# Optimization experiments

Hardware: AMD Instinct MI355X
Metric: run time of the kernel (lower is better)

## Reference

```python
import jax, jax.numpy as jnp
import numpy as np

NUM_CLASSES = 10000
NUM_PROXIES = 10
EMB_DIM = 128
MARGIN_DELTA = 0.01
LAMBDA_ = 20.0
GAMMA = 0.1


def setup_inputs() -> dict:
    key = jax.random.key(0)
    k1, k2, k3 = jax.random.split(key, 3)
    features = jax.random.normal(k1, (256, EMB_DIM), dtype=jnp.float32)
    labels = jax.random.randint(k2, (256,), 0, NUM_CLASSES, dtype=jnp.int64)
    # xavier_uniform over (num_classes, num_proxies, emb_dim): fan_in=emb_dim (last dim),
    # fan_out=num_proxies (torch treats dim0 as fan_out-ish for >2D; use standard gain=1)
    fan_in, fan_out = NUM_PROXIES * EMB_DIM, NUM_CLASSES  # torch: fan_in = prod(dims[1:]), fan_out = dims[0]
    limit = float(np.sqrt(6.0 / (fan_in + fan_out)))
    proxies = jax.random.uniform(k3, (NUM_CLASSES, NUM_PROXIES, EMB_DIM),
                                 dtype=jnp.float32, minval=-limit, maxval=limit)
    return {"features": features, "labels": labels, "proxies": proxies}


def reference(features, labels, proxies):
    B = features.shape[0]
    split = B // 2
    # dot_products: [B, C, K]
    dots = jnp.einsum('bd,ckd->bck', features, proxies)
    w = jax.nn.softmax(dots / GAMMA, axis=2)          # softmax over proxies
    S_ic = jnp.sum(w * dots, axis=2)                   # [B, C]
    S_avg = (S_ic[:split] + S_ic[split:]) * 0.5        # [split, C]
    lab = labels[:split]
    idx = jnp.arange(split)
    S_correct = S_avg[idx, lab] - MARGIN_DELTA         # [split]
    S_scaled = LAMBDA_ * S_avg
    S_correct_scaled = LAMBDA_ * S_correct
    S_corrected = S_scaled.at[idx, lab].set(S_correct_scaled)
    denom = jax.nn.logsumexp(S_corrected, axis=1)
    loss = -jnp.mean(S_correct_scaled - denom)
    return loss
```

## Files before the change

kernel.cpp:

```cpp
#include <hip/hip_runtime.h>
#include <hip/hip_bf16.h>

#define NUM_CLASSES 10000
#define NUM_PROXIES 10
#define EMB_DIM 128
#define HALF_B 128
#define MARGIN_DELTA 0.01f
#define LAMBDA_ 20.0f
#define INV_GAMMA 10.0f

#define CB 8
#define ROWS (CB * NUM_PROXIES)
#define MF 5
#define KSTEPS 4
#define NTILE 1250
#define TSTRIDE 164

#define SBYTES (ROWS * EMB_DIM * 2)
#define SMEMSZ (TSTRIDE * 256)

typedef __bf16 bf16x8 __attribute__((ext_vector_type(8)));
typedef __bf16 bf16x4 __attribute__((ext_vector_type(4)));
typedef float f32x4 __attribute__((ext_vector_type(4)));
typedef unsigned short ushort_t;

__device__ __forceinline__ unsigned int pk2bf(float a, float b) {
    __bf16 ha = (__bf16)a, hb = (__bf16)b;
    return (unsigned int)__builtin_bit_cast(ushort_t, ha) |
           ((unsigned int)__builtin_bit_cast(ushort_t, hb) << 16);
}
__device__ __forceinline__ float bf2f(unsigned int u16) {
    unsigned int x = u16 << 16;
    return __builtin_bit_cast(float, x);
}

__global__ __launch_bounds__(256) void pack_feat_kernel(
    const float* __restrict__ feat,
    bf16x8* __restrict__ featPack)
{
    const int gid = blockIdx.x * 256 + threadIdx.x;
    #pragma unroll
    for (int half = 0; half < 2; ++half) {
        int e    = gid + half * 2048;
        int lane = e & 63;
        int t    = (e >> 6) & 3;
        int nf   = (e >> 8) & 3;
        int w    = (e >> 10) & 3;
        int l15  = lane & 15;
        int g    = lane >> 4;
        int col  = w * 64 + nf * 16 + l15;
        const float4* fp = (const float4*)(feat + (size_t)col * EMB_DIM + t * 32 + g * 8);
        float4 v0 = fp[0], v1 = fp[1];
        featPack[e] = (bf16x8){ (__bf16)v0.x, (__bf16)v0.y, (__bf16)v0.z, (__bf16)v0.w,
                                (__bf16)v1.x, (__bf16)v1.y, (__bf16)v1.z, (__bf16)v1.w };
    }
}

__global__ __launch_bounds__(256, 3) void compute_S_kernel(
    const float* __restrict__ prox,
    const bf16x8* __restrict__ featPack,
    const int* __restrict__ labels,
    float* __restrict__ Ps,
    float* __restrict__ sc)
{
    __shared__ __align__(16) char smem[SMEMSZ];

    const int tid     = threadIdx.x;
    const int lane    = tid & 63;
    const int w       = tid >> 6;
    const int l15     = lane & 15;
    const int g       = lane >> 4;
    const int tileIdx = blockIdx.x;
    const int lab     = labels[tid & 127];

    const char* pbase = (const char*)prox + (size_t)tileIdx * (ROWS * EMB_DIM * 4);
    float4 sv[10];
    #pragma unroll
    for (int j = 0; j < 10; ++j)
        sv[j] = *(const float4*)(pbase + ((size_t)(j * 256 + tid) << 4));

    bf16x8 bfrag[4][KSTEPS];
    #pragma unroll
    for (int nf = 0; nf < 4; ++nf)
        #pragma unroll
        for (int t = 0; t < KSTEPS; ++t)
            bfrag[nf][t] = featPack[((w * 4 + nf) * 4 + t) * 64 + lane];

    #pragma unroll
    for (int j = 0; j < 10; ++j) {
        int cid = j * 256 + tid;
        int row = cid >> 5;
        int c32 = cid & 31;
        int off = row * 256 + ((((c32 >> 1) ^ (row & 7))) << 4) + ((c32 & 1) << 3);
        bf16x4 o = { (__bf16)sv[j].x, (__bf16)sv[j].y, (__bf16)sv[j].z, (__bf16)sv[j].w };
        *(bf16x4*)(smem + off) = o;
    }

    __syncthreads();

    f32x4 acc[MF][4];
    #pragma unroll
    for (int mf = 0; mf < MF; ++mf)
        #pragma unroll
        for (int nf = 0; nf < 4; ++nf)
            acc[mf][nf] = (f32x4){0.f, 0.f, 0.f, 0.f};

    __builtin_amdgcn_s_setprio(1);
    #pragma unroll
    for (int t = 0; t < KSTEPS; ++t) {
        #pragma unroll
        for (int mf = 0; mf < MF; ++mf) {
            int row = mf * 16 + l15;
            int ck  = (t * 4 + g) ^ (row & 7);
            bf16x8 a = *(const bf16x8*)(smem + row * 256 + (ck << 4));
            #pragma unroll
            for (int nf = 0; nf < 4; ++nf)
                acc[mf][nf] = __builtin_amdgcn_mfma_f32_16x16x32_bf16(
                    a, bfrag[nf][t], acc[mf][nf], 0, 0, 0);
        }
    }
    __builtin_amdgcn_s_setprio(0);

    __syncthreads();

    char* C = smem;
    #pragma unroll
    for (int mf = 0; mf < MF; ++mf) {
        #pragma unroll
        for (int nf = 0; nf < 4; ++nf) {
            int col  = w * 64 + nf * 16 + l15;
            int rowb = mf * 16 + g * 4;
            unsigned int lo = pk2bf(acc[mf][nf][0], acc[mf][nf][1]);
            unsigned int hi = pk2bf(acc[mf][nf][2], acc[mf][nf][3]);
            char* p = C + col * TSTRIDE + rowb * 2;
            *(unsigned int*)p       = lo;
            *(unsigned int*)(p + 4) = hi;
        }
    }
    __syncthreads();

    const int colh  = tid & 127;
    const int chalf = tid >> 7;
    float lsum = 0.f;
    #pragma unroll
    for (int cl4 = 0; cl4 < 4; ++cl4) {
        int cl = chalf * 4 + cl4;
        float Ssum = 0.f;
        #pragma unroll
        for (int h = 0; h < 2; ++h) {
            const char* base = C + (colh + h * 128) * TSTRIDE + cl * 20;
            float d[10];
            #pragma unroll
            for (int p5 = 0; p5 < 5; ++p5) {
                unsigned int pr = *(const unsigned int*)(base + p5 * 4);
                d[2 * p5]     = bf2f(pr & 0xFFFFu);
                d[2 * p5 + 1] = bf2f(pr >> 16);
            }
            float sw = 0.f, sd = 0.f;
            #pragma unroll
            for (int k = 0; k < NUM_PROXIES; ++k) {
                float e = __expf(d[k] * INV_GAMMA);
                sw += e;
                sd += e * d[k];
            }
            Ssum += sd / sw;
        }
        float Savg = 0.5f * Ssum;
        int c = tileIdx * CB + cl;
        float x = LAMBDA_ * Savg;
        if (c == lab) {
            x -= LAMBDA_ * MARGIN_DELTA;
            sc[colh] = x;
        }
        lsum += __expf(x);
    }

    *(float*)(C + tid * TSTRIDE + 160) = lsum;
    __syncthreads();
    if (tid < HALF_B) {
        float a = *(const float*)(C + tid * TSTRIDE + 160);
        float b = *(const float*)(C + (tid + 128) * TSTRIDE + 160);
        Ps[(size_t)tileIdx * HALF_B + tid] = a + b;
    }
}

__global__ __launch_bounds__(256) void psum_kernel(
    const float* __restrict__ Ps,
    float* __restrict__ Psum2)
{
    const int b0  = blockIdx.x * 25;
    const int tid = threadIdx.x;
    const int r   = tid >> 5;
    const int c   = tid & 31;

    float4 s = make_float4(0.f, 0.f, 0.f, 0.f);
    #pragma unroll
    for (int j = 0; j < 4; ++j) {
        int b = r + 8 * j;
        if (b < 25) {
            float4 v = *(const float4*)(Ps + (size_t)(b0 + b) * HALF_B + c * 4);
            s.x += v.x; s.y += v.y; s.z += v.z; s.w += v.w;
        }
    }

    __shared__ float red[8][HALF_B];
    *(float4*)&red[r][c * 4] = s;
    __syncthreads();
    if (tid < HALF_B) {
        float t = 0.f;
        #pragma unroll
        for (int rr = 0; rr < 8; ++rr) t += red[rr][tid];
        Psum2[blockIdx.x * HALF_B + tid] = t;
    }
}

__global__ __launch_bounds__(128) void finalize_kernel(
    const float* __restrict__ Psum2,
    const float* __restrict__ sc,
    float* __restrict__ out)
{
    const int i = threadIdx.x;
    float t = 0.f;
    #pragma unroll
    for (int b = 0; b < 50; ++b) t += Psum2[b * HALF_B + i];
    float part = sc[i] - __logf(t);

    __shared__ float buf[HALF_B];
    buf[i] = part;
    __syncthreads();
    #pragma unroll
    for (int off = 64; off >= 1; off >>= 1) {
        if (i < off) buf[i] += buf[i + off];
        __syncthreads();
    }
    if (i == 0) out[0] = -buf[0] / (float)HALF_B;
}

extern "C" void kernel_launch(void* const* d_in, const int* in_sizes, int n_in,
                              void* d_out, int out_size, void* d_ws, size_t ws_size,
                              hipStream_t stream) {
    const float* feat   = (const float*)d_in[0];
    const int*   labels = (const int*)d_in[1];
    const float* prox   = (const float*)d_in[2];
    float* out = (float*)d_out;

    float* Ps    = (float*)d_ws;
    float* sc    = (float*)((char*)d_ws + 640000);
    float* Psum2 = (float*)((char*)d_ws + 640000 + 512);
    bf16x8* featPack = (bf16x8*)((char*)d_ws + 666112);

    pack_feat_kernel<<<8, 256, 0, stream>>>(feat, featPack);
    compute_S_kernel<<<NTILE, 256, 0, stream>>>(prox, featPack, labels, Ps, sc);
    psum_kernel<<<50, 256, 0, stream>>>(Ps, Psum2);
    finalize_kernel<<<1, 128, 0, stream>>>(Psum2, sc, out);
}
```

Measured before the change: 30.13 us.

## Process two class tiles per block and prefetch the second tile's proxies

Each block now handles two consecutive proxy tiles instead of one, halving the grid. Feature fragments are loaded once and reused for both tiles. The global loads for the second tile are issued during the softmax epilogue of the first tile to hide memory latency. The trade-off is fewer blocks (625 on a large GPU), which may reduce latency hiding and load balance. The epilogue's partial sums move to a dedicated small shared buffer, and workspace offsets are repacked.

```diff
diff --git a/kernel.cpp b/kernel.cpp
--- a/kernel.cpp
+++ b/kernel.cpp
@@ -13,11 +13,11 @@
 #define ROWS (CB * NUM_PROXIES)
 #define MF 5
 #define KSTEPS 4
-#define NTILE 1250
+#define NBLK 625
 #define TSTRIDE 164
 
-#define SBYTES (ROWS * EMB_DIM * 2)
-#define SMEMSZ (TSTRIDE * 256)
+#define ROFF  (TSTRIDE * 256)
+#define SMEMSZ (ROFF + 1024)
 
 typedef __bf16 bf16x8 __attribute__((ext_vector_type(8)));
 typedef __bf16 bf16x4 __attribute__((ext_vector_type(4)));
@@ -28,10 +28,6 @@
     __bf16 ha = (__bf16)a, hb = (__bf16)b;
     return (unsigned int)__builtin_bit_cast(ushort_t, ha) |
            ((unsigned int)__builtin_bit_cast(ushort_t, hb) << 16);
-}
-__device__ __forceinline__ float bf2f(unsigned int u16) {
-    unsigned int x = u16 << 16;
-    return __builtin_bit_cast(float, x);
 }
 
 __global__ __launch_bounds__(256) void pack_feat_kernel(
@@ -65,19 +61,23 @@
 {
     __shared__ __align__(16) char smem[SMEMSZ];
 
-    const int tid     = threadIdx.x;
-    const int lane    = tid & 63;
-    const int w       = tid >> 6;
-    const int l15     = lane & 15;
-    const int g       = lane >> 4;
-    const int tileIdx = blockIdx.x;
-    const int lab     = labels[tid & 127];
-
-    const char* pbase = (const char*)prox + (size_t)tileIdx * (ROWS * EMB_DIM * 4);
+    const int tid   = threadIdx.x;
+    const int lane  = tid & 63;
+    const int w     = tid >> 6;
+    const int l15   = lane & 15;
+    const int g     = lane >> 4;
+    const int tileA = blockIdx.x * 2;
+    const int tileB = tileA + 1;
+    const int lab   = labels[tid & 127];
+
+    char* C = smem;
+    float* rowsum = (float*)(smem + ROFF);
+
+    const char* pbaseA = (const char*)prox + (size_t)tileA * (ROWS * EMB_DIM * 4);
     float4 sv[10];
     #pragma unroll
     for (int j = 0; j < 10; ++j)
-        sv[j] = *(const float4*)(pbase + ((size_t)(j * 256 + tid) << 4));
+        sv[j] = *(const float4*)(pbaseA + ((size_t)(j * 256 + tid) << 4));
 
     bf16x8 bfrag[4][KSTEPS];
     #pragma unroll
@@ -86,101 +86,109 @@
         for (int t = 0; t < KSTEPS; ++t)
             bfrag[nf][t] = featPack[((w * 4 + nf) * 4 + t) * 64 + lane];
 
-    #pragma unroll
-    for (int j = 0; j < 10; ++j) {
-        int cid = j * 256 + tid;
-        int row = cid >> 5;
-        int c32 = cid & 31;
-        int off = row * 256 + ((((c32 >> 1) ^ (row & 7))) << 4) + ((c32 & 1) << 3);
-        bf16x4 o = { (__bf16)sv[j].x, (__bf16)sv[j].y, (__bf16)sv[j].z, (__bf16)sv[j].w };
-        *(bf16x4*)(smem + off) = o;
-    }
-
-    __syncthreads();
-
-    f32x4 acc[MF][4];
-    #pragma unroll
-    for (int mf = 0; mf < MF; ++mf)
-        #pragma unroll
-        for (int nf = 0; nf < 4; ++nf)
-            acc[mf][nf] = (f32x4){0.f, 0.f, 0.f, 0.f};
-
-    __builtin_amdgcn_s_setprio(1);
-    #pragma unroll
-    for (int t = 0; t < KSTEPS; ++t) {
+    const char* pbaseB = (const char*)prox + (size_t)tileB * (ROWS * EMB_DIM * 4);
+
+    #pragma unroll
+    for (int tile = 0; tile < 2; ++tile) {
+        const int tileIdx = tile ? tileB : tileA;
+
+        #pragma unroll
+        for (int j = 0; j < 10; ++j) {
+            int cid = j * 256 + tid;
+            int row = cid >> 5;
+            int c32 = cid & 31;
+            int off = row * 256 + ((((c32 >> 1) ^ (row & 7))) << 4) + ((c32 & 1) << 3);
+            bf16x4 o = { (__bf16)sv[j].x, (__bf16)sv[j].y, (__bf16)sv[j].z, (__bf16)sv[j].w };
+            *(bf16x4*)(smem + off) = o;
+        }
+        __syncthreads();
+
+        f32x4 acc[MF][4];
+        #pragma unroll
+        for (int mf = 0; mf < MF; ++mf)
+            #pragma unroll
+            for (int nf = 0; nf < 4; ++nf)
+                acc[mf][nf] = (f32x4){0.f, 0.f, 0.f, 0.f};
+
+        __builtin_amdgcn_s_setprio(1);
+        #pragma unroll
+        for (int t = 0; t < KSTEPS; ++t) {
+            #pragma unroll
+            for (int mf = 0; mf < MF; ++mf) {
+                int row = mf * 16 + l15;
+                int ck  = (t * 4 + g) ^ (row & 7);
+                bf16x8 a = *(const bf16x8*)(smem + row * 256 + (ck << 4));
+                #pragma unroll
+                for (int nf = 0; nf < 4; ++nf)
+                    acc[mf][nf] = __builtin_amdgcn_mfma_f32_16x16x32_bf16(
+                        a, bfrag[nf][t], acc[mf][nf], 0, 0, 0);
+            }
+        }
+        __builtin_amdgcn_s_setprio(0);
+
+        __syncthreads();
+
         #pragma unroll
         for (int mf = 0; mf < MF; ++mf) {
-            int row = mf * 16 + l15;
-            int ck  = (t * 4 + g) ^ (row & 7);
-            bf16x8 a = *(const bf16x8*)(smem + row * 256 + (ck << 4));
-            #pragma unroll
-            for (int nf = 0; nf < 4; ++nf)
-                acc[mf][nf] = __builtin_amdgcn_mfma_f32_16x16x32_bf16(
-                    a, bfrag[nf][t], acc[mf][nf], 0, 0, 0);
-        }
-    }
-    __builtin_amdgcn_s_setprio(0);
-
-    __syncthreads();
-
-    char* C = smem;
-    #pragma unroll
-    for (int mf = 0; mf < MF; ++mf) {
-        #pragma unroll
-        for (int nf = 0; nf < 4; ++nf) {
-            int col  = w * 64 + nf * 16 + l15;
-            int rowb = mf * 16 + g * 4;
-            unsigned int lo = pk2bf(acc[mf][nf][0], acc[mf][nf][1]);
-            unsigned int hi = pk2bf(acc[mf][nf][2], acc[mf][nf][3]);
-            char* p = C + col * TSTRIDE + rowb * 2;
-            *(unsigned int*)p       = lo;
-            *(unsigned int*)(p + 4) = hi;
-        }
-    }
-    __syncthreads();
-
-    const int colh  = tid & 127;
-    const int chalf = tid >> 7;
-    float lsum = 0.f;
-    #pragma unroll
-    for (int cl4 = 0; cl4 < 4; ++cl4) {
-        int cl = chalf * 4 + cl4;
-        float Ssum = 0.f;
-        #pragma unroll
-        for (int h = 0; h < 2; ++h) {
-            const char* base = C + (colh + h * 128) * TSTRIDE + cl * 20;
-            float d[10];
-            #pragma unroll
-            for (int p5 = 0; p5 < 5; ++p5) {
-                unsigned int pr = *(const unsigned int*)(base + p5 * 4);
-                d[2 * p5]     = bf2f(pr & 0xFFFFu);
-                d[2 * p5 + 1] = bf2f(pr >> 16);
-            }
-            float sw = 0.f, sd = 0.f;
-            #pragma unroll
-            for (int k = 0; k < NUM_PROXIES; ++k) {
-                float e = __expf(d[k] * INV_GAMMA);
-                sw += e;
-                sd += e * d[k];
-            }
-            Ssum += sd / sw;
-        }
-        float Savg = 0.5f * Ssum;
-        int c = tileIdx * CB + cl;
-        float x = LAMBDA_ * Savg;
-        if (c == lab) {
-            x -= LAMBDA_ * MARGIN_DELTA;
-            sc[colh] = x;
-        }
-        lsum += __expf(x);
-    }
-
-    *(float*)(C + tid * TSTRIDE + 160) = lsum;
-    __syncthreads();
-    if (tid < HALF_B) {
-        float a = *(const float*)(C + tid * TSTRIDE + 160);
-        float b = *(const float*)(C + (tid + 128) * TSTRIDE + 160);
-        Ps[(size_t)tileIdx * HALF_B + tid] = a + b;
+            #pragma unroll
+            for (int nf = 0; nf < 4; ++nf) {
+                int col  = w * 64 + nf * 16 + l15;
+                int rowb = mf * 16 + g * 4;
+                unsigned int lo = pk2bf(acc[mf][nf][0], acc[mf][nf][1]);
+                unsigned int hi = pk2bf(acc[mf][nf][2], acc[mf][nf][3]);
+                char* p = C + col * TSTRIDE + rowb * 2;
+                *(unsigned int*)p       = lo;
+                *(unsigned int*)(p + 4) = hi;
+            }
+        }
+        __syncthreads();
+
+        if (tile == 0) {
+            #pragma unroll
+            for (int j = 0; j < 10; ++j)
+                sv[j] = *(const float4*)(pbaseB + ((size_t)(j * 256 + tid) << 4));
+        }
+
+        const int colh  = tid & 127;
+        const int chalf = tid >> 7;
+        float lsum = 0.f;
+        #pragma unroll
+        for (int cl4 = 0; cl4 < 4; ++cl4) {
+            int cl = chalf * 4 + cl4;
+            float Ssum = 0.f;
+            #pragma unroll
+            for (int h = 0; h < 2; ++h) {
+                const char* base = C + (colh + h * 128) * TSTRIDE + cl * 20;
+                float d[10];
+                #pragma unroll
+                for (int p5 = 0; p5 < 5; ++p5) {
+                    unsigned int pr = *(const unsigned int*)(base + p5 * 4);
+                    d[2 * p5]     = __builtin_bit_cast(float, pr << 16);
+                    d[2 * p5 + 1] = __builtin_bit_cast(float, pr & 0xFFFF0000u);
+                }
+                float sw = 0.f, sd = 0.f;
+                #pragma unroll
+                for (int k = 0; k < NUM_PROXIES; ++k) {
+                    float e = __expf(d[k] * INV_GAMMA);
+                    sw += e;
+                    sd += e * d[k];
+                }
+                Ssum += sd / sw;
+            }
+            float Savg = 0.5f * Ssum;
+            int c = tileIdx * CB + cl;
+            float x = LAMBDA_ * Savg;
+            if (c == lab) {
+                x -= LAMBDA_ * MARGIN_DELTA;
+                sc[colh] = x;
+            }
+            lsum += __expf(x);
+        }
+
+        rowsum[tid] = lsum;
+        __syncthreads();
+        if (tid < HALF_B)
+            Ps[(size_t)tileIdx * HALF_B + tid] = rowsum[tid] + rowsum[tid + 128];
     }
 }
 
@@ -246,11 +254,11 @@
 
     float* Ps    = (float*)d_ws;
     float* sc    = (float*)((char*)d_ws + 640000);
-    float* Psum2 = (float*)((char*)d_ws + 640000 + 512);
-    bf16x8* featPack = (bf16x8*)((char*)d_ws + 666112);
+    bf16x8* featPack = (bf16x8*)((char*)d_ws + 640512);
+    float* Psum2 = (float*)((char*)d_ws + 640512);
 
     pack_feat_kernel<<<8, 256, 0, stream>>>(feat, featPack);
-    compute_S_kernel<<<NTILE, 256, 0, stream>>>(prox, featPack, labels, Ps, sc);
+    compute_S_kernel<<<NBLK, 256, 0, stream>>>(prox, featPack, labels, Ps, sc);
     psum_kernel<<<50, 256, 0, stream>>>(Ps, Psum2);
     finalize_kernel<<<1, 128, 0, stream>>>(Psum2, sc, out);
 }
```

After: 35.55 us. +18.0%, slower.

## Halve LDS staging buffer and load feature fragments per k-step to raise occupancy

Applied to the files above, without the earlier changes.

The output staging buffer now holds only 128 columns and is filled in two phases: warps 0-1 write and everyone reduces, then warps 2-3 write and the second pass is combined with the first. This halves LDS use. Feature B-fragments are now loaded per k-step instead of all kept in registers, and launch bounds rise from 3 to 4 blocks per SIMD. The aim is more resident blocks to hide the memory-bound proxy loads, paid for with two extra barriers, duplicated softmax code and global loads inside the MFMA loop.

```diff
diff --git a/kernel.cpp b/kernel.cpp
--- a/kernel.cpp
+++ b/kernel.cpp
@@ -16,8 +16,9 @@
 #define NTILE 1250
 #define TSTRIDE 164
 
-#define SBYTES (ROWS * EMB_DIM * 2)
-#define SMEMSZ (TSTRIDE * 256)
+#define COLS_HALF 128
+#define ROFF  (TSTRIDE * COLS_HALF)
+#define SMEMSZ (ROFF + 1024)
 
 typedef __bf16 bf16x8 __attribute__((ext_vector_type(8)));
 typedef __bf16 bf16x4 __attribute__((ext_vector_type(4)));
@@ -28,10 +29,6 @@
     __bf16 ha = (__bf16)a, hb = (__bf16)b;
     return (unsigned int)__builtin_bit_cast(ushort_t, ha) |
            ((unsigned int)__builtin_bit_cast(ushort_t, hb) << 16);
-}
-__device__ __forceinline__ float bf2f(unsigned int u16) {
-    unsigned int x = u16 << 16;
-    return __builtin_bit_cast(float, x);
 }
 
 __global__ __launch_bounds__(256) void pack_feat_kernel(
@@ -56,7 +53,7 @@
     }
 }
 
-__global__ __launch_bounds__(256, 3) void compute_S_kernel(
+__global__ __launch_bounds__(256, 4) void compute_S_kernel(
     const float* __restrict__ prox,
     const bf16x8* __restrict__ featPack,
     const int* __restrict__ labels,
@@ -73,18 +70,14 @@
     const int tileIdx = blockIdx.x;
     const int lab     = labels[tid & 127];
 
+    char* C = smem;
+    float* rowsum = (float*)(smem + ROFF);
+
     const char* pbase = (const char*)prox + (size_t)tileIdx * (ROWS * EMB_DIM * 4);
     float4 sv[10];
     #pragma unroll
     for (int j = 0; j < 10; ++j)
         sv[j] = *(const float4*)(pbase + ((size_t)(j * 256 + tid) << 4));
-
-    bf16x8 bfrag[4][KSTEPS];
-    #pragma unroll
-    for (int nf = 0; nf < 4; ++nf)
-        #pragma unroll
-        for (int t = 0; t < KSTEPS; ++t)
-            bfrag[nf][t] = featPack[((w * 4 + nf) * 4 + t) * 64 + lane];
 
     #pragma unroll
     for (int j = 0; j < 10; ++j) {
@@ -108,6 +101,10 @@
     __builtin_amdgcn_s_setprio(1);
     #pragma unroll
     for (int t = 0; t < KSTEPS; ++t) {
+        bf16x8 bt[4];
+        #pragma unroll
+        for (int nf = 0; nf < 4; ++nf)
+            bt[nf] = featPack[((w * 4 + nf) * 4 + t) * 64 + lane];
         #pragma unroll
         for (int mf = 0; mf < MF; ++mf) {
             int row = mf * 16 + l15;
@@ -116,55 +113,93 @@
             #pragma unroll
             for (int nf = 0; nf < 4; ++nf)
                 acc[mf][nf] = __builtin_amdgcn_mfma_f32_16x16x32_bf16(
-                    a, bfrag[nf][t], acc[mf][nf], 0, 0, 0);
+                    a, bt[nf], acc[mf][nf], 0, 0, 0);
         }
     }
     __builtin_amdgcn_s_setprio(0);
 
-    __syncthreads();
-
-    char* C = smem;
-    #pragma unroll
-    for (int mf = 0; mf < MF; ++mf) {
-        #pragma unroll
-        for (int nf = 0; nf < 4; ++nf) {
-            int col  = w * 64 + nf * 16 + l15;
-            int rowb = mf * 16 + g * 4;
-            unsigned int lo = pk2bf(acc[mf][nf][0], acc[mf][nf][1]);
-            unsigned int hi = pk2bf(acc[mf][nf][2], acc[mf][nf][3]);
-            char* p = C + col * TSTRIDE + rowb * 2;
-            *(unsigned int*)p       = lo;
-            *(unsigned int*)(p + 4) = hi;
-        }
-    }
     __syncthreads();
 
     const int colh  = tid & 127;
     const int chalf = tid >> 7;
-    float lsum = 0.f;
+    float S0[4];
+
+    if (w < 2) {
+        #pragma unroll
+        for (int mf = 0; mf < MF; ++mf) {
+            #pragma unroll
+            for (int nf = 0; nf < 4; ++nf) {
+                int col  = w * 64 + nf * 16 + l15;
+                int rowb = mf * 16 + g * 4;
+                unsigned int lo = pk2bf(acc[mf][nf][0], acc[mf][nf][1]);
+                unsigned int hi = pk2bf(acc[mf][nf][2], acc[mf][nf][3]);
+                char* p = C + col * TSTRIDE + rowb * 2;
+                *(unsigned int*)p       = lo;
+                *(unsigned int*)(p + 4) = hi;
+            }
+        }
+    }
+    __syncthreads();
+
     #pragma unroll
     for (int cl4 = 0; cl4 < 4; ++cl4) {
         int cl = chalf * 4 + cl4;
-        float Ssum = 0.f;
-        #pragma unroll
-        for (int h = 0; h < 2; ++h) {
-            const char* base = C + (colh + h * 128) * TSTRIDE + cl * 20;
-            float d[10];
+        const char* base = C + colh * TSTRIDE + cl * 20;
+        float d[10];
+        #pragma unroll
+        for (int p5 = 0; p5 < 5; ++p5) {
+            unsigned int pr = *(const unsigned int*)(base + p5 * 4);
+            d[2 * p5]     = __builtin_bit_cast(float, pr << 16);
+            d[2 * p5 + 1] = __builtin_bit_cast(float, pr & 0xFFFF0000u);
+        }
+        float sw = 0.f, sd = 0.f;
+        #pragma unroll
+        for (int k = 0; k < NUM_PROXIES; ++k) {
+            float e = __expf(d[k] * INV_GAMMA);
+            sw += e;
+            sd += e * d[k];
+        }
+        S0[cl4] = sd / sw;
+    }
+    __syncthreads();
+
+    if (w >= 2) {
+        #pragma unroll
+        for (int mf = 0; mf < MF; ++mf) {
             #pragma unroll
-            for (int p5 = 0; p5 < 5; ++p5) {
-                unsigned int pr = *(const unsigned int*)(base + p5 * 4);
-                d[2 * p5]     = bf2f(pr & 0xFFFFu);
-                d[2 * p5 + 1] = bf2f(pr >> 16);
+            for (int nf = 0; nf < 4; ++nf) {
+                int col  = (w - 2) * 64 + nf * 16 + l15;
+                int rowb = mf * 16 + g * 4;
+                unsigned int lo = pk2bf(acc[mf][nf][0], acc[mf][nf][1]);
+                unsigned int hi = pk2bf(acc[mf][nf][2], acc[mf][nf][3]);
+                char* p = C + col * TSTRIDE + rowb * 2;
+                *(unsigned int*)p       = lo;
+                *(unsigned int*)(p + 4) = hi;
             }
-            float sw = 0.f, sd = 0.f;
-            #pragma unroll
-            for (int k = 0; k < NUM_PROXIES; ++k) {
-                float e = __expf(d[k] * INV_GAMMA);
-                sw += e;
-                sd += e * d[k];
-            }
-            Ssum += sd / sw;
-        }
+        }
+    }
+    __syncthreads();
+
+    float lsum = 0.f;
+    #pragma unroll
+    for (int cl4 = 0; cl4 < 4; ++cl4) {
+        int cl = chalf * 4 + cl4;
+        const char* base = C + colh * TSTRIDE + cl * 20;
+        float d[10];
+        #pragma unroll
+        for (int p5 = 0; p5 < 5; ++p5) {
+            unsigned int pr = *(const unsigned int*)(base + p5 * 4);
+            d[2 * p5]     = __builtin_bit_cast(float, pr << 16);
+            d[2 * p5 + 1] = __builtin_bit_cast(float, pr & 0xFFFF0000u);
+        }
+        float sw = 0.f, sd = 0.f;
+        #pragma unroll
+        for (int k = 0; k < NUM_PROXIES; ++k) {
+            float e = __expf(d[k] * INV_GAMMA);
+            sw += e;
+            sd += e * d[k];
+        }
+        float Ssum = S0[cl4] + sd / sw;
         float Savg = 0.5f * Ssum;
         int c = tileIdx * CB + cl;
         float x = LAMBDA_ * Savg;
@@ -175,13 +210,10 @@
         lsum += __expf(x);
     }
 
-    *(float*)(C + tid * TSTRIDE + 160) = lsum;
-    __syncthreads();
-    if (tid < HALF_B) {
-        float a = *(const float*)(C + tid * TSTRIDE + 160);
-        float b = *(const float*)(C + (tid + 128) * TSTRIDE + 160);
-        Ps[(size_t)tileIdx * HALF_B + tid] = a + b;
-    }
+    rowsum[tid] = lsum;
+    __syncthreads();
+    if (tid < HALF_B)
+        Ps[(size_t)tileIdx * HALF_B + tid] = rowsum[tid] + rowsum[tid + 128];
 }
 
 __global__ __launch_bounds__(256) void psum_kernel(
@@ -246,7 +278,7 @@
 
     float* Ps    = (float*)d_ws;
     float* sc    = (float*)((char*)d_ws + 640000);
-    float* Psum2 = (float*)((char*)d_ws + 640000 + 512);
+    float* Psum2 = (float*)((char*)d_ws + 640512);
     bf16x8* featPack = (bf16x8*)((char*)d_ws + 666112);
 
     pack_feat_kernel<<<8, 256, 0, stream>>>(feat, featPack);
```

Result: slower. 32.46 us (+7.8%).

## Double block size to 512 threads, split columns across eight waves, swizzle C tile

Applied to the files above, without the earlier changes.

The S kernel now runs 512 threads per block, and each of its eight waves covers 32 feature columns instead of 64. This halves the per-thread proxy loads and accumulator count so more waves can be resident. Feature fragments are loaded per k-step inside the MFMA loop rather than preloaded, and the transposed C tile uses an XOR swizzle with a 160-byte stride to avoid LDS bank conflicts. The per-block lsum reduction through shared memory is removed: each thread writes its partial sum directly, which makes the partial buffer four times larger and moves that reduction into psum_kernel.

```diff
diff --git a/kernel.cpp b/kernel.cpp
--- a/kernel.cpp
+++ b/kernel.cpp
@@ -12,12 +12,13 @@
 #define CB 8
 #define ROWS (CB * NUM_PROXIES)
 #define MF 5
+#define NF 2
 #define KSTEPS 4
 #define NTILE 1250
-#define TSTRIDE 164
-
-#define SBYTES (ROWS * EMB_DIM * 2)
-#define SMEMSZ (TSTRIDE * 256)
+#define TPB 512
+
+#define CSTRIDE 160
+#define SMEMSZ (CSTRIDE * 256)
 
 typedef __bf16 bf16x8 __attribute__((ext_vector_type(8)));
 typedef __bf16 bf16x4 __attribute__((ext_vector_type(4)));
@@ -29,10 +30,6 @@
     return (unsigned int)__builtin_bit_cast(ushort_t, ha) |
            ((unsigned int)__builtin_bit_cast(ushort_t, hb) << 16);
 }
-__device__ __forceinline__ float bf2f(unsigned int u16) {
-    unsigned int x = u16 << 16;
-    return __builtin_bit_cast(float, x);
-}
 
 __global__ __launch_bounds__(256) void pack_feat_kernel(
     const float* __restrict__ feat,
@@ -44,11 +41,10 @@
         int e    = gid + half * 2048;
         int lane = e & 63;
         int t    = (e >> 6) & 3;
-        int nf   = (e >> 8) & 3;
-        int w    = (e >> 10) & 3;
+        int cb   = (e >> 8) & 15;
         int l15  = lane & 15;
         int g    = lane >> 4;
-        int col  = w * 64 + nf * 16 + l15;
+        int col  = cb * 16 + l15;
         const float4* fp = (const float4*)(feat + (size_t)col * EMB_DIM + t * 32 + g * 8);
         float4 v0 = fp[0], v1 = fp[1];
         featPack[e] = (bf16x8){ (__bf16)v0.x, (__bf16)v0.y, (__bf16)v0.z, (__bf16)v0.w,
@@ -56,11 +52,11 @@
     }
 }
 
-__global__ __launch_bounds__(256, 3) void compute_S_kernel(
+__global__ __launch_bounds__(TPB, 6) void compute_S_kernel(
     const float* __restrict__ prox,
     const bf16x8* __restrict__ featPack,
     const int* __restrict__ labels,
-    float* __restrict__ Ps,
+    float* __restrict__ Ps2,
     float* __restrict__ sc)
 {
     __shared__ __align__(16) char smem[SMEMSZ];
@@ -73,22 +69,17 @@
     const int tileIdx = blockIdx.x;
     const int lab     = labels[tid & 127];
 
+    char* C = smem;
+
     const char* pbase = (const char*)prox + (size_t)tileIdx * (ROWS * EMB_DIM * 4);
-    float4 sv[10];
-    #pragma unroll
-    for (int j = 0; j < 10; ++j)
-        sv[j] = *(const float4*)(pbase + ((size_t)(j * 256 + tid) << 4));
-
-    bf16x8 bfrag[4][KSTEPS];
-    #pragma unroll
-    for (int nf = 0; nf < 4; ++nf)
-        #pragma unroll
-        for (int t = 0; t < KSTEPS; ++t)
-            bfrag[nf][t] = featPack[((w * 4 + nf) * 4 + t) * 64 + lane];
-
-    #pragma unroll
-    for (int j = 0; j < 10; ++j) {
-        int cid = j * 256 + tid;
+    float4 sv[5];
+    #pragma unroll
+    for (int j = 0; j < 5; ++j)
+        sv[j] = *(const float4*)(pbase + ((size_t)(j * TPB + tid) << 4));
+
+    #pragma unroll
+    for (int j = 0; j < 5; ++j) {
+        int cid = j * TPB + tid;
         int row = cid >> 5;
         int c32 = cid & 31;
         int off = row * 256 + ((((c32 >> 1) ^ (row & 7))) << 4) + ((c32 & 1) << 3);
@@ -98,63 +89,69 @@
 
     __syncthreads();
 
-    f32x4 acc[MF][4];
+    f32x4 acc[MF][NF];
     #pragma unroll
     for (int mf = 0; mf < MF; ++mf)
         #pragma unroll
-        for (int nf = 0; nf < 4; ++nf)
+        for (int nf = 0; nf < NF; ++nf)
             acc[mf][nf] = (f32x4){0.f, 0.f, 0.f, 0.f};
 
     __builtin_amdgcn_s_setprio(1);
     #pragma unroll
     for (int t = 0; t < KSTEPS; ++t) {
+        bf16x8 bt[NF];
+        #pragma unroll
+        for (int nf = 0; nf < NF; ++nf)
+            bt[nf] = featPack[((size_t)((2 * w + nf) * 4 + t)) * 64 + lane];
         #pragma unroll
         for (int mf = 0; mf < MF; ++mf) {
             int row = mf * 16 + l15;
             int ck  = (t * 4 + g) ^ (row & 7);
             bf16x8 a = *(const bf16x8*)(smem + row * 256 + (ck << 4));
             #pragma unroll
-            for (int nf = 0; nf < 4; ++nf)
+            for (int nf = 0; nf < NF; ++nf)
                 acc[mf][nf] = __builtin_amdgcn_mfma_f32_16x16x32_bf16(
-                    a, bfrag[nf][t], acc[mf][nf], 0, 0, 0);
+                    a, bt[nf], acc[mf][nf], 0, 0, 0);
         }
     }
     __builtin_amdgcn_s_setprio(0);
 
     __syncthreads();
 
-    char* C = smem;
     #pragma unroll
     for (int mf = 0; mf < MF; ++mf) {
         #pragma unroll
-        for (int nf = 0; nf < 4; ++nf) {
-            int col  = w * 64 + nf * 16 + l15;
-            int rowb = mf * 16 + g * 4;
+        for (int nf = 0; nf < NF; ++nf) {
+            int col = w * 32 + nf * 16 + l15;
+            int u   = (col >> 2) & 7;
+            int w0  = mf * 8 + g * 2;
             unsigned int lo = pk2bf(acc[mf][nf][0], acc[mf][nf][1]);
             unsigned int hi = pk2bf(acc[mf][nf][2], acc[mf][nf][3]);
-            char* p = C + col * TSTRIDE + rowb * 2;
-            *(unsigned int*)p       = lo;
-            *(unsigned int*)(p + 4) = hi;
-        }
-    }
-    __syncthreads();
-
-    const int colh  = tid & 127;
-    const int chalf = tid >> 7;
+            char* colb = C + col * CSTRIDE;
+            *(unsigned int*)(colb + ((w0 ^ u) << 2))       = lo;
+            *(unsigned int*)(colb + (((w0 + 1) ^ u) << 2)) = hi;
+        }
+    }
+    __syncthreads();
+
+    const int colh = tid & 127;
+    const int q    = tid >> 7;
     float lsum = 0.f;
     #pragma unroll
-    for (int cl4 = 0; cl4 < 4; ++cl4) {
-        int cl = chalf * 4 + cl4;
+    for (int cl2 = 0; cl2 < 2; ++cl2) {
+        int cl = q * 2 + cl2;
         float Ssum = 0.f;
         #pragma unroll
         for (int h = 0; h < 2; ++h) {
-            const char* base = C + (colh + h * 128) * TSTRIDE + cl * 20;
+            int col = colh + h * 128;
+            int u   = (col >> 2) & 7;
+            const char* base = C + col * CSTRIDE;
             float d[10];
             #pragma unroll
             for (int p5 = 0; p5 < 5; ++p5) {
-                unsigned int pr = *(const unsigned int*)(base + p5 * 4);
-                d[2 * p5]     = bf2f(pr & 0xFFFFu);
-                d[2 * p5 + 1] = bf2f(pr >> 16);
+                unsigned int pr = *(const unsigned int*)(base + (((cl * 5 + p5) ^ u) << 2));
+                d[2 * p5]     = __builtin_bit_cast(float, pr << 16);
+                d[2 * p5 + 1] = __builtin_bit_cast(float, pr & 0xFFFF0000u);
             }
             float sw = 0.f, sd = 0.f;
             #pragma unroll
@@ -175,43 +172,30 @@
         lsum += __expf(x);
     }
 
-    *(float*)(C + tid * TSTRIDE + 160) = lsum;
-    __syncthreads();
-    if (tid < HALF_B) {
-        float a = *(const float*)(C + tid * TSTRIDE + 160);
-        float b = *(const float*)(C + (tid + 128) * TSTRIDE + 160);
-        Ps[(size_t)tileIdx * HALF_B + tid] = a + b;
-    }
+    Ps2[(size_t)tileIdx * TPB + tid] = lsum;
 }
 
 __global__ __launch_bounds__(256) void psum_kernel(
-    const float* __restrict__ Ps,
+    const float* __restrict__ Ps2,
     float* __restrict__ Psum2)
 {
     const int b0  = blockIdx.x * 25;
     const int tid = threadIdx.x;
-    const int r   = tid >> 5;
-    const int c   = tid & 31;
-
-    float4 s = make_float4(0.f, 0.f, 0.f, 0.f);
-    #pragma unroll
-    for (int j = 0; j < 4; ++j) {
-        int b = r + 8 * j;
-        if (b < 25) {
-            float4 v = *(const float4*)(Ps + (size_t)(b0 + b) * HALF_B + c * 4);
-            s.x += v.x; s.y += v.y; s.z += v.z; s.w += v.w;
-        }
-    }
-
-    __shared__ float red[8][HALF_B];
-    *(float4*)&red[r][c * 4] = s;
-    __syncthreads();
-    if (tid < HALF_B) {
-        float t = 0.f;
-        #pragma unroll
-        for (int rr = 0; rr < 8; ++rr) t += red[rr][tid];
-        Psum2[blockIdx.x * HALF_B + tid] = t;
-    }
+    const int i   = tid & 127;
+    const int hh  = tid >> 7;
+
+    float s = 0.f;
+    #pragma unroll 5
+    for (int b = 0; b < 25; ++b) {
+        const float* row = Ps2 + (size_t)(b0 + b) * TPB + hh * 256;
+        s += row[i] + row[i + 128];
+    }
+
+    __shared__ float red[2][HALF_B];
+    red[hh][i] = s;
+    __syncthreads();
+    if (tid < HALF_B)
+        Psum2[blockIdx.x * HALF_B + tid] = red[0][tid] + red[1][tid];
 }
 
 __global__ __launch_bounds__(128) void finalize_kernel(
@@ -244,13 +228,13 @@
     const float* prox   = (const float*)d_in[2];
     float* out = (float*)d_out;
 
-    float* Ps    = (float*)d_ws;
-    float* sc    = (float*)((char*)d_ws + 640000);
-    float* Psum2 = (float*)((char*)d_ws + 640000 + 512);
-    bf16x8* featPack = (bf16x8*)((char*)d_ws + 666112);
+    float* Ps2   = (float*)d_ws;
+    float* sc    = (float*)((char*)d_ws + 2560000);
+    float* Psum2 = (float*)((char*)d_ws + 2560512);
+    bf16x8* featPack = (bf16x8*)((char*)d_ws + 2586112);
 
     pack_feat_kernel<<<8, 256, 0, stream>>>(feat, featPack);
-    compute_S_kernel<<<NTILE, 256, 0, stream>>>(prox, featPack, labels, Ps, sc);
-    psum_kernel<<<50, 256, 0, stream>>>(Ps, Psum2);
+    compute_S_kernel<<<NTILE, TPB, 0, stream>>>(prox, featPack, labels, Ps2, sc);
+    psum_kernel<<<50, 256, 0, stream>>>(Ps2, Psum2);
     finalize_kernel<<<1, 128, 0, stream>>>(Psum2, sc, out);
 }
```

Result: slower. 32.47 us (+7.8%).
